# Performance work log

Hardware: AMD Instinct MI355X
Metric: run time of the kernel (lower is better)

The kernel has to match this reference:

```python
import jax, jax.numpy as jnp
import numpy as np


def quantize(weights):
    # per-output-channel threshold alpha = mean |w| over in_features
    alpha = jnp.mean(jnp.abs(weights), axis=1, keepdims=True)  # (out, 1)
    return jnp.where(weights > alpha, 1.0,
                     jnp.where(weights < -alpha, -1.0, 0.0)).astype(weights.dtype)


def setup_inputs() -> dict:
    key = jax.random.key(0)
    k1, k2 = jax.random.split(key)
    B, S, DIN, DOUT = 4, 2048, 4096, 4096
    x = jax.random.normal(k1, (B, S, DIN), dtype=jnp.float32)
    weight = jax.random.normal(k2, (DOUT, DIN), dtype=jnp.float32)
    scale = jnp.ones((DOUT, 1), dtype=jnp.float32)
    bias = jnp.zeros((DOUT,), dtype=jnp.float32)
    return {"x": x, "weight": weight, "scale": scale, "bias": bias}


def reference(x, weight, scale, bias):
    # training-mode path with straight-through estimator
    q = quantize(weight)
    qw = jax.lax.stop_gradient(q) + weight - jax.lax.stop_gradient(weight)
    scaled_weight = qw * scale  # (out, in)
    # F.linear: x @ W^T + b
    out = jnp.einsum('bsi,oi->bso', x, scaled_weight) + bias
    return out
```

## Files before the change

### kernel.cpp

```cpp
#include <hip/hip_runtime.h>
#include <hip/hip_bf16.h>
#include <stdint.h>

#define DIN   4096
#define DOUT  4096
#define MTOT  8192

#define BK    64
#define NKT   (DIN / BK)

typedef int i32x4 __attribute__((ext_vector_type(4)));

__device__ __forceinline__ void glds16(const void* g, void* l) {
  __builtin_amdgcn_global_load_lds(
      (__attribute__((address_space(1))) void*)g,
      (__attribute__((address_space(3))) void*)l, 16, 0, 0);
}

__global__ __launch_bounds__(256) void quant_fused(
    const float* __restrict__ W, int8_t* __restrict__ QW,
    const float* __restrict__ X, int8_t* __restrict__ XQ,
    float* __restrict__ XS) {
  const int t = threadIdx.x;

  if (blockIdx.x < DOUT) {
    const int row = blockIdx.x;
    const float* wr = W + (size_t)row * DIN;

    float4 v[4];
    double s = 0.0;
#pragma unroll
    for (int j = 0; j < 4; ++j) {
      v[j] = reinterpret_cast<const float4*>(wr)[j * 256 + t];
      s += (double)fabsf(v[j].x) + (double)fabsf(v[j].y) +
           (double)fabsf(v[j].z) + (double)fabsf(v[j].w);
    }
#pragma unroll
    for (int off = 32; off > 0; off >>= 1) s += __shfl_down(s, off, 64);

    __shared__ double ssum[4];
    __shared__ float salpha;
    if ((t & 63) == 0) ssum[t >> 6] = s;
    __syncthreads();
    if (t == 0)
      salpha = (float)((ssum[0] + ssum[1] + ssum[2] + ssum[3]) / (double)DIN);
    __syncthreads();
    const float alpha = salpha;

    int* qo = reinterpret_cast<int*>(QW + (size_t)row * DIN);
#pragma unroll
    for (int j = 0; j < 4; ++j) {
      int q0 = v[j].x > alpha ? 1 : (v[j].x < -alpha ? -1 : 0);
      int q1 = v[j].y > alpha ? 1 : (v[j].y < -alpha ? -1 : 0);
      int q2 = v[j].z > alpha ? 1 : (v[j].z < -alpha ? -1 : 0);
      int q3 = v[j].w > alpha ? 1 : (v[j].w < -alpha ? -1 : 0);
      qo[j * 256 + t] =
          (q0 & 0xff) | ((q1 & 0xff) << 8) | ((q2 & 0xff) << 16) | ((q3 & 0xff) << 24);
    }
  } else {
    const int row = blockIdx.x - DOUT;
    const float* xr = X + (size_t)row * DIN;

    float4 v[4];
    float mx = 0.f;
#pragma unroll
    for (int j = 0; j < 4; ++j) {
      v[j] = reinterpret_cast<const float4*>(xr)[j * 256 + t];
      mx = fmaxf(mx, fmaxf(fmaxf(fabsf(v[j].x), fabsf(v[j].y)),
                           fmaxf(fabsf(v[j].z), fabsf(v[j].w))));
    }
#pragma unroll
    for (int off = 32; off > 0; off >>= 1) mx = fmaxf(mx, __shfl_down(mx, off, 64));

    __shared__ float smax[4];
    __shared__ float sinv, ssc;
    if ((t & 63) == 0) smax[t >> 6] = mx;
    __syncthreads();
    if (t == 0) {
      float rm = fmaxf(fmaxf(smax[0], smax[1]), fmaxf(smax[2], smax[3]));
      sinv = rm > 0.f ? 127.f / rm : 0.f;
      ssc  = rm > 0.f ? rm / 127.f : 0.f;
    }
    __syncthreads();
    const float inv = sinv;
    if (t == 0) XS[row] = ssc;

    int* qo = reinterpret_cast<int*>(XQ + (size_t)row * DIN);
#pragma unroll
    for (int j = 0; j < 4; ++j) {
      int q0 = (int)rintf(v[j].x * inv);
      int q1 = (int)rintf(v[j].y * inv);
      int q2 = (int)rintf(v[j].z * inv);
      int q3 = (int)rintf(v[j].w * inv);
      qo[j * 256 + t] =
          (q0 & 0xff) | ((q1 & 0xff) << 8) | ((q2 & 0xff) << 16) | ((q3 & 0xff) << 24);
    }
  }
}

__global__ __launch_bounds__(1024, 4) void gemm256_i8(
    const int8_t* __restrict__ XQ, const int8_t* __restrict__ QW,
    const float* __restrict__ XS, const float* __restrict__ scale,
    const float* __restrict__ bias, float* __restrict__ out) {
  __shared__ int8_t As[2][16384];
  __shared__ int8_t Bs[2][16384];

  const int t = threadIdx.x;
  const int lane = t & 63;
  const int wid = t >> 6;
  const int wr = wid >> 2, wc = wid & 3;
  const int m0 = blockIdx.x * 256;
  const int n0 = blockIdx.y * 256;

  const int8_t* ag = XQ + (size_t)m0 * DIN;
  const int8_t* bg = QW + (size_t)n0 * DIN;

  i32x4 acc[4][4] = {};
  i32x4 a[4], b[4];

  const int r = lane & 15, kq = lane >> 4;
  const int srow = t >> 2;
  const int scol = ((t & 3) ^ ((srow >> 1) & 3)) * 16;

#define ISSUE_T(Tt_, isb_) do {                                                 \
    const int T_ = (Tt_);                                                       \
    if (T_ < NKT) {                                                             \
      const int bf_ = T_ & 1;                                                   \
      const int8_t* gb_ = (isb_) ? bg : ag;                                     \
      int8_t* lb_ = (isb_) ? &Bs[bf_][0] : &As[bf_][0];                         \
      glds16(gb_ + (size_t)srow * DIN + T_ * 64 + scol, lb_ + t * 16);          \
    }                                                                           \
  } while (0)

#define READA(buf_) do {                                                        \
    _Pragma("unroll")                                                           \
    for (int mi = 0; mi < 4; ++mi) {                                            \
      const int row_ = wr * 64 + mi * 16 + r;                                   \
      a[mi] = *reinterpret_cast<const i32x4*>(                                  \
          &As[buf_][row_ * 64 + (kq ^ ((row_ >> 1) & 3)) * 16]);                \
    }                                                                           \
  } while (0)

#define READB(buf_) do {                                                        \
    _Pragma("unroll")                                                           \
    for (int ni = 0; ni < 4; ++ni) {                                            \
      const int row_ = wc * 64 + ni * 16 + r;                                   \
      b[ni] = *reinterpret_cast<const i32x4*>(                                  \
          &Bs[buf_][row_ * 64 + (kq ^ ((row_ >> 1) & 3)) * 16]);                \
    }                                                                           \
  } while (0)

#define MMA8(nh_) do {                                                          \
    _Pragma("unroll")                                                           \
    for (int mi = 0; mi < 4; ++mi) {                                            \
      _Pragma("unroll")                                                         \
      for (int ni = 0; ni < 2; ++ni) {                                          \
        acc[mi][(nh_) * 2 + ni] =                                               \
            __builtin_amdgcn_mfma_i32_16x16x64_i8(                              \
                a[mi], b[(nh_) * 2 + ni], acc[mi][(nh_) * 2 + ni], 0, 0, 0);    \
      }                                                                         \
    }                                                                           \
  } while (0)

#define BAR() __builtin_amdgcn_s_barrier()

#define TILE(T_, buf_) do {                                                     \
             \
    READA(buf_);                                                                \
    READB(buf_);                                                                \
    ISSUE_T((T_) + 1, 0);                                                       \
    MMA8(0);                                                                    \
    BAR();                                                                      \
                   \
    ISSUE_T((T_) + 2, 1);                                                       \
    MMA8(1);                                                                    \
    if ((T_) < NKT - 2)                                                         \
      asm volatile("s_waitcnt vmcnt(1)" ::: "memory");                          \
    else                                                                        \
      asm volatile("s_waitcnt vmcnt(0)" ::: "memory");                          \
    BAR();                                                                      \
  } while (0)

  ISSUE_T(0, 0); ISSUE_T(0, 1); ISSUE_T(1, 1);
  asm volatile("s_waitcnt vmcnt(1)" ::: "memory");
  __builtin_amdgcn_s_barrier();

  for (int T = 0; T < NKT; T += 2) {
    TILE(T, 0);
    TILE(T + 1, 1);
  }

  const int q4 = lane >> 4;
#pragma unroll
  for (int ni = 0; ni < 4; ++ni) {
    const int col = n0 + wc * 64 + ni * 16 + r;
    const float sc = scale[col];
    const float bs = bias[col];
#pragma unroll
    for (int mi = 0; mi < 4; ++mi) {
      const int row = m0 + wr * 64 + mi * 16 + q4 * 4;
      const float4 xs4 = *reinterpret_cast<const float4*>(&XS[row]);
      out[(size_t)(row + 0) * DOUT + col] = (float)acc[mi][ni][0] * (xs4.x * sc) + bs;
      out[(size_t)(row + 1) * DOUT + col] = (float)acc[mi][ni][1] * (xs4.y * sc) + bs;
      out[(size_t)(row + 2) * DOUT + col] = (float)acc[mi][ni][2] * (xs4.z * sc) + bs;
      out[(size_t)(row + 3) * DOUT + col] = (float)acc[mi][ni][3] * (xs4.w * sc) + bs;
    }
  }
#undef ISSUE_T
#undef READA
#undef READB
#undef MMA8
#undef BAR
#undef TILE
}

extern "C" void kernel_launch(void* const* d_in, const int* in_sizes, int n_in,
                              void* d_out, int out_size, void* d_ws, size_t ws_size,
                              hipStream_t stream) {
  const float* X     = (const float*)d_in[0];
  const float* W     = (const float*)d_in[1];
  const float* scale = (const float*)d_in[2];
  const float* bias  = (const float*)d_in[3];
  float* out = (float*)d_out;

  int8_t* QW = (int8_t*)d_ws;
  int8_t* XQ = (int8_t*)d_ws + (size_t)DOUT * DIN;
  float*  XS = (float*)((int8_t*)d_ws + (size_t)DOUT * DIN + (size_t)MTOT * DIN);

  quant_fused<<<DOUT + MTOT, 256, 0, stream>>>(W, QW, X, XQ, XS);
  dim3 grid(MTOT / 256, DOUT / 256);
  gemm256_i8<<<grid, 1024, 0, stream>>>(XQ, QW, XS, scale, bias, out);
}
```

Measured before the change: 194.4 us.

## Switch int8 GEMM to 4-stage LDS ring with two-tile-ahead prefetch

Grows the A and B shared-memory buffers from two stages to four, giving 128 KB of LDS per block. Both A and B loads for tile T+2 are now issued while tile T is computed, instead of staggering A and B loads across two half-tiles. Each tile now uses a single barrier, cutting the synchronisation count in half. The cost is doubled LDS footprint, which limits blocks per CU and therefore occupancy.

```diff
diff --git a/kernel.cpp b/kernel.cpp
--- a/kernel.cpp
+++ b/kernel.cpp
@@ -102,8 +102,8 @@
     const int8_t* __restrict__ XQ, const int8_t* __restrict__ QW,
     const float* __restrict__ XS, const float* __restrict__ scale,
     const float* __restrict__ bias, float* __restrict__ out) {
-  __shared__ int8_t As[2][16384];
-  __shared__ int8_t Bs[2][16384];
+  __shared__ int8_t As[4][16384];
+  __shared__ int8_t Bs[4][16384];
 
   const int t = threadIdx.x;
   const int lane = t & 63;
@@ -122,72 +122,71 @@
   const int srow = t >> 2;
   const int scol = ((t & 3) ^ ((srow >> 1) & 3)) * 16;
 
-#define ISSUE_T(Tt_, isb_) do {                                                 \
+#define ISSUE_A(Tt_, ab_) do {                                                  \
     const int T_ = (Tt_);                                                       \
-    if (T_ < NKT) {                                                             \
-      const int bf_ = T_ & 1;                                                   \
-      const int8_t* gb_ = (isb_) ? bg : ag;                                     \
-      int8_t* lb_ = (isb_) ? &Bs[bf_][0] : &As[bf_][0];                         \
-      glds16(gb_ + (size_t)srow * DIN + T_ * 64 + scol, lb_ + t * 16);          \
-    }                                                                           \
-  } while (0)
-
-#define READA(buf_) do {                                                        \
+    if (T_ < NKT)                                                               \
+      glds16(ag + (size_t)srow * DIN + T_ * 64 + scol, &As[ab_][0] + t * 16);   \
+  } while (0)
+
+#define ISSUE_B(Tt_, bb_) do {                                                  \
+    const int T_ = (Tt_);                                                       \
+    if (T_ < NKT)                                                               \
+      glds16(bg + (size_t)srow * DIN + T_ * 64 + scol, &Bs[bb_][0] + t * 16);   \
+  } while (0)
+
+#define READA(ab_) do {                                                         \
     _Pragma("unroll")                                                           \
     for (int mi = 0; mi < 4; ++mi) {                                            \
       const int row_ = wr * 64 + mi * 16 + r;                                   \
       a[mi] = *reinterpret_cast<const i32x4*>(                                  \
-          &As[buf_][row_ * 64 + (kq ^ ((row_ >> 1) & 3)) * 16]);                \
+          &As[ab_][row_ * 64 + (kq ^ ((row_ >> 1) & 3)) * 16]);                 \
     }                                                                           \
   } while (0)
 
-#define READB(buf_) do {                                                        \
+#define READB(bb_) do {                                                         \
     _Pragma("unroll")                                                           \
     for (int ni = 0; ni < 4; ++ni) {                                            \
       const int row_ = wc * 64 + ni * 16 + r;                                   \
       b[ni] = *reinterpret_cast<const i32x4*>(                                  \
-          &Bs[buf_][row_ * 64 + (kq ^ ((row_ >> 1) & 3)) * 16]);                \
+          &Bs[bb_][row_ * 64 + (kq ^ ((row_ >> 1) & 3)) * 16]);                 \
     }                                                                           \
   } while (0)
 
-#define MMA8(nh_) do {                                                          \
+#define MMA16() do {                                                            \
     _Pragma("unroll")                                                           \
     for (int mi = 0; mi < 4; ++mi) {                                            \
       _Pragma("unroll")                                                         \
-      for (int ni = 0; ni < 2; ++ni) {                                          \
-        acc[mi][(nh_) * 2 + ni] =                                               \
-            __builtin_amdgcn_mfma_i32_16x16x64_i8(                              \
-                a[mi], b[(nh_) * 2 + ni], acc[mi][(nh_) * 2 + ni], 0, 0, 0);    \
+      for (int ni = 0; ni < 4; ++ni) {                                          \
+        acc[mi][ni] = __builtin_amdgcn_mfma_i32_16x16x64_i8(                    \
+            a[mi], b[ni], acc[mi][ni], 0, 0, 0);                                \
       }                                                                         \
     }                                                                           \
   } while (0)
 
 #define BAR() __builtin_amdgcn_s_barrier()
 
-#define TILE(T_, buf_) do {                                                     \
-             \
-    READA(buf_);                                                                \
-    READB(buf_);                                                                \
-    ISSUE_T((T_) + 1, 0);                                                       \
-    MMA8(0);                                                                    \
-    BAR();                                                                      \
-                   \
-    ISSUE_T((T_) + 2, 1);                                                       \
-    MMA8(1);                                                                    \
+#define TILE(T_, ab_) do {                                                      \
+    READA(ab_);                                                                 \
+    READB(ab_);                                                                 \
+    ISSUE_A((T_) + 2, ((ab_) + 2) & 3);                                         \
+    ISSUE_B((T_) + 2, ((ab_) + 2) & 3);                                         \
+    MMA16();                                                                    \
     if ((T_) < NKT - 2)                                                         \
-      asm volatile("s_waitcnt vmcnt(1)" ::: "memory");                          \
+      asm volatile("s_waitcnt vmcnt(2)" ::: "memory");                          \
     else                                                                        \
       asm volatile("s_waitcnt vmcnt(0)" ::: "memory");                          \
     BAR();                                                                      \
   } while (0)
 
-  ISSUE_T(0, 0); ISSUE_T(0, 1); ISSUE_T(1, 1);
-  asm volatile("s_waitcnt vmcnt(1)" ::: "memory");
+  ISSUE_A(0, 0); ISSUE_B(0, 0); ISSUE_A(1, 1); ISSUE_B(1, 1);
+  asm volatile("s_waitcnt vmcnt(2)" ::: "memory");
   __builtin_amdgcn_s_barrier();
 
-  for (int T = 0; T < NKT; T += 2) {
+  for (int T = 0; T < NKT; T += 4) {
     TILE(T, 0);
     TILE(T + 1, 1);
+    TILE(T + 2, 2);
+    TILE(T + 3, 3);
   }
 
   const int q4 = lane >> 4;
@@ -206,10 +205,11 @@
       out[(size_t)(row + 3) * DOUT + col] = (float)acc[mi][ni][3] * (xs4.w * sc) + bs;
     }
   }
-#undef ISSUE_T
+#undef ISSUE_A
+#undef ISSUE_B
 #undef READA
 #undef READB
-#undef MMA8
+#undef MMA16
 #undef BAR
 #undef TILE
 }
```

New measurement: 214.6 us. 1.1x slower.
